# Performance work log

Measured on AMD Instinct MI355X. Metric: run time of the kernel, lower is better.

## Reference

```python
import jax, jax.numpy as jnp
import numpy as np

EPROJS = 512
ODIM = 600
DLAYERS = 2
DUNITS = 512
EMBED_DIM = 512
JOINT_DIM = 512
BLANK = 0


def setup_inputs() -> dict:
    key = jax.random.key(0)
    ks = jax.random.split(key, 20)
    B, T, U = 16, 200, 64
    s_d = 1.0 / np.sqrt(DUNITS)
    s_e = 1.0 / np.sqrt(EPROJS)
    s_j = 1.0 / np.sqrt(JOINT_DIM)
    inp = {
        "hs_pad": jax.random.normal(ks[0], (B, T, EPROJS), dtype=jnp.float32),
        "ys_in_pad": jax.random.randint(ks[1], (B, U), 0, ODIM),
        "embed_table": jax.random.normal(ks[2], (ODIM, EMBED_DIM), dtype=jnp.float32).at[BLANK].set(0.0),
        # LSTMCell layer 0: input EMBED_DIM -> DUNITS (gates i,f,g,o stacked => 4*DUNITS)
        "W_ih0": jax.random.uniform(ks[3], (4 * DUNITS, EMBED_DIM), minval=-s_d, maxval=s_d),
        "W_hh0": jax.random.uniform(ks[4], (4 * DUNITS, DUNITS), minval=-s_d, maxval=s_d),
        "b_ih0": jax.random.uniform(ks[5], (4 * DUNITS,), minval=-s_d, maxval=s_d),
        "b_hh0": jax.random.uniform(ks[6], (4 * DUNITS,), minval=-s_d, maxval=s_d),
        # LSTMCell layer 1: DUNITS -> DUNITS
        "W_ih1": jax.random.uniform(ks[7], (4 * DUNITS, DUNITS), minval=-s_d, maxval=s_d),
        "W_hh1": jax.random.uniform(ks[8], (4 * DUNITS, DUNITS), minval=-s_d, maxval=s_d),
        "b_ih1": jax.random.uniform(ks[9], (4 * DUNITS,), minval=-s_d, maxval=s_d),
        "b_hh1": jax.random.uniform(ks[10], (4 * DUNITS,), minval=-s_d, maxval=s_d),
        # joint network
        "W_enc": jax.random.uniform(ks[11], (JOINT_DIM, EPROJS), minval=-s_e, maxval=s_e),
        "b_enc": jax.random.uniform(ks[12], (JOINT_DIM,), minval=-s_e, maxval=s_e),
        "W_dec": jax.random.uniform(ks[13], (JOINT_DIM, DUNITS), minval=-s_d, maxval=s_d),
        "W_out": jax.random.uniform(ks[14], (ODIM, JOINT_DIM), minval=-s_j, maxval=s_j),
        "b_out": jax.random.uniform(ks[15], (ODIM,), minval=-s_j, maxval=s_j),
    }
    return inp


def _lstm_cell(x, h, c, W_ih, W_hh, b_ih, b_hh):
    gates = x @ W_ih.T + b_ih + h @ W_hh.T + b_hh  # (B, 4*D)
    i, f, g, o = jnp.split(gates, 4, axis=-1)
    c_new = jax.nn.sigmoid(f) * c + jax.nn.sigmoid(i) * jnp.tanh(g)
    h_new = jax.nn.sigmoid(o) * jnp.tanh(c_new)
    return h_new, c_new


def _decode(eys, W_ih0, W_hh0, b_ih0, b_hh0, W_ih1, W_hh1, b_ih1, b_hh1):
    # eys: (B, U, E). Sequential 2-layer LSTM over U via scan.
    B = eys.shape[0]
    z = jnp.zeros((B, DUNITS), dtype=eys.dtype)
    carry0 = (z, z, z, z)  # h0, c0, h1, c1

    def step(carry, ey):
        h0, c0, h1, c1 = carry
        h0, c0 = _lstm_cell(ey, h0, c0, W_ih0, W_hh0, b_ih0, b_hh0)
        h1, c1 = _lstm_cell(h0, h1, c1, W_ih1, W_hh1, b_ih1, b_hh1)
        return (h0, c0, h1, c1), h1

    _, h_dec = jax.lax.scan(step, carry0, jnp.swapaxes(eys, 0, 1))  # (U, B, D)
    return jnp.swapaxes(h_dec, 0, 1)  # (B, U, D)


def reference(hs_pad, ys_in_pad, embed_table, W_ih0, W_hh0, b_ih0, b_hh0,
              W_ih1, W_hh1, b_ih1, b_hh1, W_enc, b_enc, W_dec, W_out, b_out):
    eys = embed_table[ys_in_pad]  # (B, U, E); dropout = identity at p=0
    h_dec = _decode(eys, W_ih0, W_hh0, b_ih0, b_hh0, W_ih1, W_hh1, b_ih1, b_hh1)
    # Joint: project BEFORE broadcasting (thin GEMMs), then broadcast-add.
    enc_p = hs_pad @ W_enc.T + b_enc            # (B, T, J)
    dec_p = h_dec @ W_dec.T                     # (B, U, J)
    z = jnp.tanh(enc_p[:, :, None, :] + dec_p[:, None, :, :])  # (B, T, U, J)
    return z @ W_out.T + b_out                  # (B, T, U, odim)
```

## Files before the change

kernel.cpp:

```cpp
#include <hip/hip_runtime.h>
#include <hip/hip_bf16.h>
#include <stdint.h>

#define DEVI __device__ __forceinline__

typedef unsigned short u16;
typedef __attribute__((ext_vector_type(8))) short short8;
typedef __attribute__((ext_vector_type(4))) float f32x4;
typedef __attribute__((ext_vector_type(16))) float f32x16;

DEVI u16 f2bf(float f) {
  union { float f; uint32_t u; } v; v.f = f;
  return (u16)((v.u + 0x7fffu + ((v.u >> 16) & 1u)) >> 16);
}
DEVI float tanh_c(float x) {
  float e = __expf(x + x);
  float r = __builtin_amdgcn_rcpf(e + 1.0f);
  return __builtin_fmaf(-2.0f, r, 1.0f);
}
DEVI float sigm(float x) { return __builtin_amdgcn_rcpf(1.0f + __expf(-x)); }
DEVI uint32_t tj2(float a, float b) {
  float ea = __expf(a + a), eb = __expf(b + b);
  float ta = __builtin_fmaf(-2.0f, __builtin_amdgcn_rcpf(ea + 1.0f), 1.0f);
  float tb = __builtin_fmaf(-2.0f, __builtin_amdgcn_rcpf(eb + 1.0f), 1.0f);
  union { __hip_bfloat162 h; uint32_t u; } cv;
  cv.h = __float22bfloat162_rn(make_float2(ta, tb));
  return cv.u;
}

__global__ void prep_kernel(
    const float* __restrict__ W_ih0, const float* __restrict__ W_hh0,
    const float* __restrict__ W_ih1, const float* __restrict__ W_hh1,
    const float* __restrict__ W_enc, const float* __restrict__ W_dec,
    const float* __restrict__ W_out, const float* __restrict__ embed,
    const float* __restrict__ hs_pad,
    const float* __restrict__ b_ih0, const float* __restrict__ b_hh0,
    const float* __restrict__ b_ih1, const float* __restrict__ b_hh1,
    const float* __restrict__ b_out,
    u16* __restrict__ Wih0b, u16* __restrict__ Whh0b,
    u16* __restrict__ Wih1b, u16* __restrict__ Whh1b,
    u16* __restrict__ Wencb, u16* __restrict__ Wdecb,
    u16* __restrict__ embedb, u16* __restrict__ hsb,
    u16* __restrict__ Wshufb,
    float* __restrict__ bsum0, float* __restrict__ bsum1, float* __restrict__ boutp)
{
  const int c1 = 1048576, c2 = 2097152, c3 = 3145728, c4 = 4194304;
  const int c5 = 4456448, c6 = 4718592, c7 = 5025792, c8 = 6664192;
  const int c9 = 6991872, c10 = 6993920, c11 = 6995968, c12 = 6996608;
  for (int i = blockIdx.x * blockDim.x + threadIdx.x; i < c12; i += gridDim.x * blockDim.x) {
    if (i < c1)       Wih0b[i]      = f2bf(W_ih0[i]);
    else if (i < c2)  Whh0b[i - c1] = f2bf(W_hh0[i - c1]);
    else if (i < c3)  Wih1b[i - c2] = f2bf(W_ih1[i - c2]);
    else if (i < c4)  Whh1b[i - c3] = f2bf(W_hh1[i - c3]);
    else if (i < c5)  Wencb[i - c4] = f2bf(W_enc[i - c4]);
    else if (i < c6)  Wdecb[i - c5] = f2bf(W_dec[i - c5]);
    else if (i < c7)  embedb[i - c6] = f2bf(embed[i - c6]);
    else if (i < c8)  hsb[i - c7]   = f2bf(hs_pad[i - c7]);
    else if (i < c9) {
      int e = i - c8;
      int kc = e / 10240, r = e % 10240;
      int tile = r >> 9, r2 = r & 511;
      int lane = r2 >> 3, ii = r2 & 7;
      int n = tile * 32 + (lane & 31);
      int k = kc * 16 + ((lane >> 5) << 3) + ii;
      Wshufb[e] = (n < 600) ? f2bf(W_out[n * 512 + k]) : (u16)0;
    }
    else if (i < c10) { int n = i - c9;  bsum0[n] = b_ih0[n] + b_hh0[n]; }
    else if (i < c11) { int n = i - c10; bsum1[n] = b_ih1[n] + b_hh1[n]; }
    else              { int n = i - c11; boutp[n] = (n < 600) ? b_out[n] : 0.0f; }
  }
}

__global__ __launch_bounds__(256) void gemm_bf16(
    const u16* __restrict__ A, const u16* __restrict__ B,
    const int* __restrict__ ys, const float* __restrict__ bias,
    float* __restrict__ out, int N, int mode)
{
  int tid = threadIdx.x, wv = tid >> 6, l = tid & 63;
  int m0 = blockIdx.x * 64, n0 = blockIdx.y * 64;
  int row = m0 + wv * 16 + (l & 15);
  const u16* arow;
  if (mode == 1) { int uu = row >> 4, bb = row & 15; arow = A + (size_t)ys[bb * 64 + uu] * 512; }
  else           arow = A + (size_t)row * 512;
  int kof = (l >> 4) * 8;
  arow += kof;
  const u16* br = B + (size_t)(n0 + (l & 15)) * 512 + kof;
  f32x4 a0 = {0.f,0.f,0.f,0.f}, a1 = a0, a2 = a0, a3 = a0;
  for (int kk = 0; kk < 512; kk += 32) {
    short8 av = *(const short8*)(arow + kk);
    short8 b0 = *(const short8*)(br + kk);
    short8 b1 = *(const short8*)(br + 8192 + kk);
    short8 b2 = *(const short8*)(br + 16384 + kk);
    short8 b3 = *(const short8*)(br + 24576 + kk);
    a0 = __builtin_amdgcn_mfma_f32_16x16x32_bf16(av, b0, a0, 0, 0, 0);
    a1 = __builtin_amdgcn_mfma_f32_16x16x32_bf16(av, b1, a1, 0, 0, 0);
    a2 = __builtin_amdgcn_mfma_f32_16x16x32_bf16(av, b2, a2, 0, 0, 0);
    a3 = __builtin_amdgcn_mfma_f32_16x16x32_bf16(av, b3, a3, 0, 0, 0);
  }
  int col = l & 15, rb = m0 + wv * 16 + (l >> 4) * 4;
  f32x4 accs[4] = {a0, a1, a2, a3};
#pragma unroll
  for (int g = 0; g < 4; ++g) {
    int n = n0 + g * 16 + col;
    float bs = bias ? bias[n] : 0.0f;
#pragma unroll
    for (int i2 = 0; i2 < 4; ++i2)
      out[(size_t)(rb + i2) * N + n] = accs[g][i2] + bs;
  }
}

#define L0WG 32
#define NWGT 96

DEVI short8 ald16(const u16* p) {
  union { unsigned long long q[2]; short8 v; } u;
  u.q[0] = __hip_atomic_load((unsigned long long*)p,       __ATOMIC_RELAXED, __HIP_MEMORY_SCOPE_AGENT);
  u.q[1] = __hip_atomic_load((unsigned long long*)(p + 4), __ATOMIC_RELAXED, __HIP_MEMORY_SCOPE_AGENT);
  return u.v;
}
DEVI void waitflags(const int* f0, const int* f1, int n0, int n1) {
  if (threadIdx.x < 64) {
    int l = threadIdx.x;
    for (;;) {
      int a = __hip_atomic_load((int*)(f0 + (l & 31) * 16), __ATOMIC_RELAXED, __HIP_MEMORY_SCOPE_AGENT);
      int b = __hip_atomic_load((int*)(f1 + l * 16),        __ATOMIC_RELAXED, __HIP_MEMORY_SCOPE_AGENT);
      if (__all(a >= n0 && b >= n1)) break;
      __builtin_amdgcn_s_sleep(1);
    }
    __builtin_amdgcn_fence(__ATOMIC_ACQUIRE, "agent");
  }
  __syncthreads();
}
DEVI void postflag(int* slot, int val) {
  __syncthreads();
  if (threadIdx.x == 0) {
    asm volatile("s_waitcnt vmcnt(0)" ::: "memory");
    __hip_atomic_store(slot, val, __ATOMIC_RELAXED, __HIP_MEMORY_SCOPE_AGENT);
  }
}
DEVI const u16* haddr(const u16* base, int slot, int k, int b) {
  return base + slot * 8192 + (k >> 4) * 256 + b * 16 + (k & 15);
}
DEVI void hstore(u16* base, int idx, u16 mine, int tid) {
  int other = __shfl_xor((int)mine, 1);
  if (!(tid & 1)) {
    uint32_t pkv = (uint32_t)mine | (((uint32_t)other & 0xffffu) << 16);
    __hip_atomic_store((uint32_t*)(base + idx), pkv, __ATOMIC_RELAXED, __HIP_MEMORY_SCOPE_AGENT);
  }
}

__global__ __launch_bounds__(256) void lstm_kernel(
    const float* __restrict__ Xg0,
    const u16* __restrict__ Whh0, const u16* __restrict__ Wih1, const u16* __restrict__ Whh1,
    const float* __restrict__ bsum1,
    u16* __restrict__ h0b, u16* __restrict__ h1b,
    u16* __restrict__ Hdec,
    int* __restrict__ flags0, int* __restrict__ flags1)
{
  __shared__ float red[16][256];
  const int bid = blockIdx.x, tid = threadIdx.x;
  const int wv = tid >> 6, l = tid & 63;
  const int lb = l & 15, kof = (l >> 4) * 8;
  const int drb = (l >> 4) * 4;

  if (bid < L0WG) {
    const int be = tid >> 4, je = tid & 15, jg = (bid << 4) + je;
    short8 breg[16];
#pragma unroll
    for (int g = 0; g < 4; ++g) {
      const u16* bp = Whh0 + (size_t)(g * 512 + bid * 16 + lb) * 512 + wv * 128 + kof;
#pragma unroll
      for (int ks = 0; ks < 4; ++ks)
        breg[g * 4 + ks] = *(const short8*)(bp + ks * 32);
    }
    float c0 = 0.f;
    for (int t = 0; t < 64; ++t) {
      const float* xg = Xg0 + (size_t)((t << 4) + be) * 2048 + jg;
      float x0 = xg[0], x1 = xg[512], x2 = xg[1024], x3 = xg[1536];
      waitflags(flags0, flags1, t, (t > 7) ? (t - 7) : 0);
      const int rs = (t + 7) & 7;
      f32x4 g0 = {0.f,0.f,0.f,0.f}, g1 = g0, g2 = g0, g3 = g0;
#pragma unroll
      for (int ks = 0; ks < 4; ++ks) {
        int kk = wv * 128 + ks * 32 + kof;
        short8 av = ald16(haddr(h0b, rs, kk, lb));
        g0 = __builtin_amdgcn_mfma_f32_16x16x32_bf16(av, breg[0 * 4 + ks], g0, 0, 0, 0);
        g1 = __builtin_amdgcn_mfma_f32_16x16x32_bf16(av, breg[1 * 4 + ks], g1, 0, 0, 0);
        g2 = __builtin_amdgcn_mfma_f32_16x16x32_bf16(av, breg[2 * 4 + ks], g2, 0, 0, 0);
        g3 = __builtin_amdgcn_mfma_f32_16x16x32_bf16(av, breg[3 * 4 + ks], g3, 0, 0, 0);
      }
      f32x4 gs[4] = {g0, g1, g2, g3};
#pragma unroll
      for (int g = 0; g < 4; ++g)
#pragma unroll
        for (int i2 = 0; i2 < 4; ++i2)
          red[wv * 4 + g][(drb + i2) * 16 + lb] = gs[g][i2];
      __syncthreads();
      {
        float s0 = 0, s1 = 0, s2 = 0, s3 = 0;
#pragma unroll
        for (int v2 = 0; v2 < 4; ++v2) {
          s0 += red[v2 * 4 + 0][be * 16 + je]; s1 += red[v2 * 4 + 1][be * 16 + je];
          s2 += red[v2 * 4 + 2][be * 16 + je]; s3 += red[v2 * 4 + 3][be * 16 + je];
        }
        float gi = s0 + x0, gf = s1 + x1, gg = s2 + x2, go = s3 + x3;
        float I = sigm(gi), F = sigm(gf), G = tanh_c(gg), O = sigm(go);
        c0 = F * c0 + I * G;
        float h0 = O * tanh_c(c0);
        hstore(h0b, ((t & 7) * 32 + bid) * 256 + (tid & ~1), f2bf(h0), tid);
      }
      postflag(flags0 + bid * 16, t + 1);
    }
  } else {
    const int v = bid - L0WG;
    const u16* base0 = (wv < 2) ? Wih1 : Whh1;
    const int kbase = (wv & 1) * 256;
    short8 breg[16];
#pragma unroll
    for (int tt = 0; tt < 2; ++tt) {
      int c = tt * 16 + lb, gate = c >> 3, du = c & 7;
      const u16* bp = base0 + (size_t)(gate * 512 + v * 8 + du) * 512 + kbase + kof;
#pragma unroll
      for (int ks = 0; ks < 8; ++ks)
        breg[tt * 8 + ks] = *(const short8*)(bp + ks * 32);
    }
    float bs0 = 0, bs1 = 0, bs2 = 0, bs3 = 0, c1 = 0.f;
    if (tid < 128) {
      int du = tid & 7, ju = v * 8 + du;
      bs0 = bsum1[ju]; bs1 = bsum1[512 + ju]; bs2 = bsum1[1024 + ju]; bs3 = bsum1[1536 + ju];
    }
    for (int t = 0; t < 64; ++t) {
      waitflags(flags0, flags1, t + 1, t);
      const u16* hsrc = (wv < 2) ? (h0b + (t & 7) * 8192) : (h1b + ((t + 7) & 7) * 8192);
      f32x4 g0 = {0.f,0.f,0.f,0.f}, g1 = g0;
#pragma unroll
      for (int ks = 0; ks < 8; ++ks) {
        int kk = kbase + ks * 32 + kof;
        short8 av = ald16(hsrc + (kk >> 4) * 256 + lb * 16 + (kk & 15));
        g0 = __builtin_amdgcn_mfma_f32_16x16x32_bf16(av, breg[0 * 8 + ks], g0, 0, 0, 0);
        g1 = __builtin_amdgcn_mfma_f32_16x16x32_bf16(av, breg[1 * 8 + ks], g1, 0, 0, 0);
      }
#pragma unroll
      for (int i2 = 0; i2 < 4; ++i2) {
        red[wv * 2 + 0][(drb + i2) * 16 + lb] = g0[i2];
        red[wv * 2 + 1][(drb + i2) * 16 + lb] = g1[i2];
      }
      __syncthreads();
      u16 hb = 0; int be = 0, ju = 0;
      if (tid < 128) {
        be = tid >> 3; int du = tid & 7; ju = v * 8 + du;
        float sg[4] = {bs0, bs1, bs2, bs3};
#pragma unroll
        for (int g = 0; g < 4; ++g) {
          int c = g * 8 + du, tt = c >> 4, cc = c & 15;
          float acc = 0.f;
#pragma unroll
          for (int w2 = 0; w2 < 4; ++w2) acc += red[w2 * 2 + tt][be * 16 + cc];
          sg[g] += acc;
        }
        float I = sigm(sg[0]), F = sigm(sg[1]), G = tanh_c(sg[2]), O = sigm(sg[3]);
        c1 = F * c1 + I * G;
        float h1v = O * tanh_c(c1);
        hb = f2bf(h1v);
        int idx = ((t & 7) * 32 + (ju >> 4)) * 256 + be * 16 + (ju & 15);
        hstore(h1b, idx & ~1, hb, tid);
      }
      postflag(flags1 + v * 16, t + 1);
      if (tid < 128) Hdec[(size_t)((t << 4) + be) * 512 + ju] = hb;
    }
  }
}

__global__ __launch_bounds__(256) void joint_kernel(
    const float* __restrict__ enc_p,
    const float* __restrict__ dec_p,
    const u16* __restrict__ Wshuf,
    const float* __restrict__ boutp,
    float* __restrict__ out)
{
  __shared__ int4 wlds[2][1280];
  __shared__ int4 zlds[2][256];
  int bid = blockIdx.x;
  int b = bid / 400, rem = bid % 400;
  int tb = rem / 8, rem2 = rem % 8;
  int ub = rem2 >> 1, nh = rem2 & 1;
  int tid = threadIdx.x, wv = tid >> 6, l = tid & 63;
  int mv = wv >> 1, nv = wv & 1;
  int ln31 = l & 31, lh = l >> 5;
  const int tile0 = nv * 5;
  f32x16 acc[5];
#pragma unroll
  for (int j = 0; j < 5; ++j) {
    float bv = boutp[nh * 320 + (tile0 + j) * 32 + ln31];
#pragma unroll
    for (int g = 0; g < 16; ++g) acc[j][g] = bv;
  }
  int zr = tid & 63, zg = tid >> 6;
  const float* er = enc_p + (size_t)(b * 200 + tb * 4 + (zr >> 4)) * 512 + zg * 8;
  const float* dr = dec_p + (size_t)((ub * 16 + (zr & 15)) * 16 + b) * 512 + zg * 8;
  const int zslot = ((zg >> 1) * 2 + (zr >> 5)) * 64 + ((zg & 1) << 5) + (zr & 31);
  const int4* gW = (const int4*)Wshuf;
  const int nhof = nh * 640;
  const int L0 = tid, L1 = 256 + tid, L2 = 512 + tid + ((tid >= 128) ? 640 : 0),
            L3 = 1408 + tid, L4 = 1664 + tid;
  const int S2 = 512 + tid;

  {
    int4 w0 = gW[nhof + L0], w1 = gW[nhof + L1], w2 = gW[nhof + L2],
         w3 = gW[nhof + L3], w4 = gW[nhof + L4];
    float4 e0 = *(const float4*)(er),     e1 = *(const float4*)(er + 4);
    float4 d0 = *(const float4*)(dr),     d1 = *(const float4*)(dr + 4);
    int4 pk;
    pk.x = (int)tj2(e0.x + d0.x, e0.y + d0.y);
    pk.y = (int)tj2(e0.z + d0.z, e0.w + d0.w);
    pk.z = (int)tj2(e1.x + d1.x, e1.y + d1.y);
    pk.w = (int)tj2(e1.z + d1.z, e1.w + d1.w);
    zlds[0][zslot] = pk;
    wlds[0][tid] = w0; wlds[0][256 + tid] = w1; wlds[0][S2] = w2;
    wlds[0][768 + tid] = w3; wlds[0][1024 + tid] = w4;
    __syncthreads();
  }

  for (int c = 0; c < 16; ++c) {
    const int cur = c & 1, nxt = cur ^ 1;
    const bool pf = (c < 15);
    int4 w0, w1, w2, w3, w4;
    float4 e0, e1, d0, d1;
    if (pf) {
      const int cb = (c + 1) * 2560 + nhof;
      w0 = gW[cb + L0]; w1 = gW[cb + L1]; w2 = gW[cb + L2];
      w3 = gW[cb + L3]; w4 = gW[cb + L4];
      int k0 = (c + 1) * 32;
      e0 = *(const float4*)(er + k0);     e1 = *(const float4*)(er + k0 + 4);
      d0 = *(const float4*)(dr + k0);     d1 = *(const float4*)(dr + k0 + 4);
    }
#pragma unroll
    for (int ks = 0; ks < 2; ++ks) {
      short8 aA = *(const short8*)&zlds[cur][(ks * 2 + mv) * 64 + l];
#pragma unroll
      for (int j = 0; j < 5; ++j) {
        short8 bw = *(const short8*)&wlds[cur][ks * 640 + (tile0 + j) * 64 + l];
        acc[j] = __builtin_amdgcn_mfma_f32_32x32x16_bf16(aA, bw, acc[j], 0, 0, 0);
      }
    }
    if (pf) {
      wlds[nxt][tid] = w0; wlds[nxt][256 + tid] = w1; wlds[nxt][S2] = w2;
      wlds[nxt][768 + tid] = w3; wlds[nxt][1024 + tid] = w4;
      int4 pk;
      pk.x = (int)tj2(e0.x + d0.x, e0.y + d0.y);
      pk.y = (int)tj2(e0.z + d0.z, e0.w + d0.w);
      pk.z = (int)tj2(e1.x + d1.x, e1.y + d1.y);
      pk.w = (int)tj2(e1.z + d1.z, e1.w + d1.w);
      zlds[nxt][zslot] = pk;
    }
    __syncthreads();
  }

#pragma unroll
  for (int j = 0; j < 5; ++j) {
    int n = nh * 320 + (tile0 + j) * 32 + ln31;
    if (n < 600) {
      int rbase = mv * 32 + 4 * lh;
#pragma unroll
      for (int g = 0; g < 16; ++g) {
        int r = rbase + (g & 3) + ((g >> 2) << 3);
        int tt = tb * 4 + (r >> 4), uu = ub * 16 + (r & 15);
        __builtin_nontemporal_store(
            acc[j][g], &out[(size_t)((b * 200 + tt) * 64 + uu) * 600 + n]);
      }
    }
  }
}

extern "C" void kernel_launch(void* const* d_in, const int* in_sizes, int n_in,
                              void* d_out, int out_size, void* d_ws, size_t ws_size,
                              hipStream_t stream) {
  const float* hs_pad = (const float*)d_in[0];
  const int*   ys     = (const int*)d_in[1];
  const float* embed  = (const float*)d_in[2];
  const float* W_ih0  = (const float*)d_in[3];
  const float* W_hh0  = (const float*)d_in[4];
  const float* b_ih0  = (const float*)d_in[5];
  const float* b_hh0  = (const float*)d_in[6];
  const float* W_ih1  = (const float*)d_in[7];
  const float* W_hh1  = (const float*)d_in[8];
  const float* b_ih1  = (const float*)d_in[9];
  const float* b_hh1  = (const float*)d_in[10];
  const float* W_enc  = (const float*)d_in[11];
  const float* b_enc  = (const float*)d_in[12];
  const float* W_dec  = (const float*)d_in[13];
  const float* W_out  = (const float*)d_in[14];
  const float* b_out  = (const float*)d_in[15];
  float* out = (float*)d_out;

  uint8_t* ws = (uint8_t*)d_ws;
  size_t off = 0;
  auto alloc = [&](size_t bytes) -> void* {
    void* p = ws + off;
    off = (off + bytes + 255) & ~(size_t)255;
    return p;
  };
  int* flags0   = (int*)alloc(2048);
  int* flags1   = (int*)alloc(4096);
  u16* h0buf    = (u16*)alloc(8 * 32 * 256 * 2);
  u16* h1buf    = (u16*)alloc(8 * 32 * 256 * 2);
  u16* Hdec     = (u16*)alloc(64 * 16 * 512 * 2);
  float* Xg0    = (float*)alloc(1024 * 2048 * 4);
  float* enc_p  = (float*)alloc(3200 * 512 * 4);
  float* dec_p  = (float*)alloc(1024 * 512 * 4);
  u16* Wih0b    = (u16*)alloc(2048 * 512 * 2);
  u16* Whh0b    = (u16*)alloc(2048 * 512 * 2);
  u16* Wih1b    = (u16*)alloc(2048 * 512 * 2);
  u16* Whh1b    = (u16*)alloc(2048 * 512 * 2);
  u16* Wencb    = (u16*)alloc(512 * 512 * 2);
  u16* Wdecb    = (u16*)alloc(512 * 512 * 2);
  u16* embedb   = (u16*)alloc(600 * 512 * 2);
  u16* hsb      = (u16*)alloc(3200 * 512 * 2);
  u16* Wshufb   = (u16*)alloc(32 * 20 * 64 * 8 * 2);
  float* bsum0  = (float*)alloc(2048 * 4);
  float* bsum1  = (float*)alloc(2048 * 4);
  float* boutp  = (float*)alloc(640 * 4);

  (void)hipMemsetAsync(d_ws, 0, 2048 + 4096 + 131072 + 131072, stream);

  prep_kernel<<<2048, 256, 0, stream>>>(
      W_ih0, W_hh0, W_ih1, W_hh1, W_enc, W_dec, W_out, embed, hs_pad,
      b_ih0, b_hh0, b_ih1, b_hh1, b_out,
      Wih0b, Whh0b, Wih1b, Whh1b, Wencb, Wdecb, embedb, hsb, Wshufb,
      bsum0, bsum1, boutp);

  dim3 g1(16, 32);
  gemm_bf16<<<g1, 256, 0, stream>>>(embedb, Wih0b, ys, bsum0, Xg0, 2048, 1);
  dim3 g2(50, 8);
  gemm_bf16<<<g2, 256, 0, stream>>>(hsb, Wencb, nullptr, b_enc, enc_p, 512, 0);
  lstm_kernel<<<NWGT, 256, 0, stream>>>(Xg0, Whh0b, Wih1b, Whh1b, bsum1,
                                        h0buf, h1buf, Hdec, flags0, flags1);
  dim3 g3(16, 8);
  gemm_bf16<<<g3, 256, 0, stream>>>(Hdec, Wdecb, nullptr, nullptr, dec_p, 512, 0);
  joint_kernel<<<6400, 256, 0, stream>>>(enc_p, dec_p, Wshufb, boutp, out);
}
```

Before: 604.9 us.

## Replace flag-based LSTM synchronization with tagged hidden-state words in full-length ring

The persistent LSTM kernel no longer posts and polls per-workgroup flags. Each packed bf16 pair of the hidden state is now written as a 64-bit word carrying its timestep tag, and consumers spin until every loaded word has the expected tag. This removes the separate flag round trip, the acquire fence and one barrier per step from the recurrent critical path. In exchange the h buffers are twice as wide, hold all 65 timesteps instead of an 8-slot ring, and need a larger memset, and correctness relies on each 64-bit atomic store being seen whole.

```diff
diff --git a/kernel.cpp b/kernel.cpp
--- a/kernel.cpp
+++ b/kernel.cpp
@@ -5,6 +5,7 @@
 #define DEVI __device__ __forceinline__
 
 typedef unsigned short u16;
+typedef unsigned long long u64;
 typedef __attribute__((ext_vector_type(8))) short short8;
 typedef __attribute__((ext_vector_type(4))) float f32x4;
 typedef __attribute__((ext_vector_type(16))) float f32x16;
@@ -112,40 +113,24 @@
 #define L0WG 32
 #define NWGT 96
 
-DEVI short8 ald16(const u16* p) {
-  union { unsigned long long q[2]; short8 v; } u;
-  u.q[0] = __hip_atomic_load((unsigned long long*)p,       __ATOMIC_RELAXED, __HIP_MEMORY_SCOPE_AGENT);
-  u.q[1] = __hip_atomic_load((unsigned long long*)(p + 4), __ATOMIC_RELAXED, __HIP_MEMORY_SCOPE_AGENT);
-  return u.v;
-}
-DEVI void waitflags(const int* f0, const int* f1, int n0, int n1) {
-  if (threadIdx.x < 64) {
-    int l = threadIdx.x;
-    for (;;) {
-      int a = __hip_atomic_load((int*)(f0 + (l & 31) * 16), __ATOMIC_RELAXED, __HIP_MEMORY_SCOPE_AGENT);
-      int b = __hip_atomic_load((int*)(f1 + l * 16),        __ATOMIC_RELAXED, __HIP_MEMORY_SCOPE_AGENT);
-      if (__all(a >= n0 && b >= n1)) break;
-      __builtin_amdgcn_s_sleep(1);
-    }
-    __builtin_amdgcn_fence(__ATOMIC_ACQUIRE, "agent");
-  }
-  __syncthreads();
-}
-DEVI void postflag(int* slot, int val) {
-  __syncthreads();
-  if (threadIdx.x == 0) {
-    asm volatile("s_waitcnt vmcnt(0)" ::: "memory");
-    __hip_atomic_store(slot, val, __ATOMIC_RELAXED, __HIP_MEMORY_SCOPE_AGENT);
-  }
-}
-DEVI const u16* haddr(const u16* base, int slot, int k, int b) {
-  return base + slot * 8192 + (k >> 4) * 256 + b * 16 + (k & 15);
-}
-DEVI void hstore(u16* base, int idx, u16 mine, int tid) {
+DEVI bool tagld4(const u64* p, uint32_t tag, short8* out) {
+  u64 q0 = __hip_atomic_load(p + 0, __ATOMIC_RELAXED, __HIP_MEMORY_SCOPE_AGENT);
+  u64 q1 = __hip_atomic_load(p + 1, __ATOMIC_RELAXED, __HIP_MEMORY_SCOPE_AGENT);
+  u64 q2 = __hip_atomic_load(p + 2, __ATOMIC_RELAXED, __HIP_MEMORY_SCOPE_AGENT);
+  u64 q3 = __hip_atomic_load(p + 3, __ATOMIC_RELAXED, __HIP_MEMORY_SCOPE_AGENT);
+  union { int4 d; short8 s; } u;
+  u.d = make_int4((int)(uint32_t)q0, (int)(uint32_t)q1,
+                  (int)(uint32_t)q2, (int)(uint32_t)q3);
+  *out = u.s;
+  return ((uint32_t)(q0 >> 32) == tag) & ((uint32_t)(q1 >> 32) == tag)
+       & ((uint32_t)(q2 >> 32) == tag) & ((uint32_t)(q3 >> 32) == tag);
+}
+DEVI void hst64(u64* base, int idx, u16 mine, int tid, uint32_t tag) {
   int other = __shfl_xor((int)mine, 1);
   if (!(tid & 1)) {
-    uint32_t pkv = (uint32_t)mine | (((uint32_t)other & 0xffffu) << 16);
-    __hip_atomic_store((uint32_t*)(base + idx), pkv, __ATOMIC_RELAXED, __HIP_MEMORY_SCOPE_AGENT);
+    u64 v = ((u64)tag << 32) |
+            (u64)(uint32_t)((uint32_t)mine | (((uint32_t)other & 0xffffu) << 16));
+    __hip_atomic_store(base + idx, v, __ATOMIC_RELAXED, __HIP_MEMORY_SCOPE_AGENT);
   }
 }
 
@@ -153,15 +138,15 @@
     const float* __restrict__ Xg0,
     const u16* __restrict__ Whh0, const u16* __restrict__ Wih1, const u16* __restrict__ Whh1,
     const float* __restrict__ bsum1,
-    u16* __restrict__ h0b, u16* __restrict__ h1b,
-    u16* __restrict__ Hdec,
-    int* __restrict__ flags0, int* __restrict__ flags1)
+    u64* __restrict__ h0r, u64* __restrict__ h1r,
+    u16* __restrict__ Hdec)
 {
   __shared__ float red[16][256];
   const int bid = blockIdx.x, tid = threadIdx.x;
   const int wv = tid >> 6, l = tid & 63;
   const int lb = l & 15, kof = (l >> 4) * 8;
   const int drb = (l >> 4) * 4;
+  const int pof = ((kof >> 4)) * 128 + lb * 8 + ((kof & 8) >> 1);
 
   if (bid < L0WG) {
     const int be = tid >> 4, je = tid & 15, jg = (bid << 4) + je;
@@ -173,22 +158,38 @@
       for (int ks = 0; ks < 4; ++ks)
         breg[g * 4 + ks] = *(const short8*)(bp + ks * 32);
     }
+    const int koff = wv * 8 * 128 + pof;
     float c0 = 0.f;
     for (int t = 0; t < 64; ++t) {
       const float* xg = Xg0 + (size_t)((t << 4) + be) * 2048 + jg;
       float x0 = xg[0], x1 = xg[512], x2 = xg[1024], x3 = xg[1536];
-      waitflags(flags0, flags1, t, (t > 7) ? (t - 7) : 0);
-      const int rs = (t + 7) & 7;
+      const u64* hp = h0r + (size_t)t * 4096 + koff;
+      short8 av0, av1, av2, av3;
+      for (;;) {
+        bool ok = tagld4(hp +   0, (uint32_t)t, &av0);
+        ok &=     tagld4(hp + 256, (uint32_t)t, &av1);
+        ok &=     tagld4(hp + 512, (uint32_t)t, &av2);
+        ok &=     tagld4(hp + 768, (uint32_t)t, &av3);
+        if (__all(ok)) break;
+        __builtin_amdgcn_s_sleep(1);
+      }
       f32x4 g0 = {0.f,0.f,0.f,0.f}, g1 = g0, g2 = g0, g3 = g0;
-#pragma unroll
-      for (int ks = 0; ks < 4; ++ks) {
-        int kk = wv * 128 + ks * 32 + kof;
-        short8 av = ald16(haddr(h0b, rs, kk, lb));
-        g0 = __builtin_amdgcn_mfma_f32_16x16x32_bf16(av, breg[0 * 4 + ks], g0, 0, 0, 0);
-        g1 = __builtin_amdgcn_mfma_f32_16x16x32_bf16(av, breg[1 * 4 + ks], g1, 0, 0, 0);
-        g2 = __builtin_amdgcn_mfma_f32_16x16x32_bf16(av, breg[2 * 4 + ks], g2, 0, 0, 0);
-        g3 = __builtin_amdgcn_mfma_f32_16x16x32_bf16(av, breg[3 * 4 + ks], g3, 0, 0, 0);
-      }
+      g0 = __builtin_amdgcn_mfma_f32_16x16x32_bf16(av0, breg[0],  g0, 0, 0, 0);
+      g1 = __builtin_amdgcn_mfma_f32_16x16x32_bf16(av0, breg[4],  g1, 0, 0, 0);
+      g2 = __builtin_amdgcn_mfma_f32_16x16x32_bf16(av0, breg[8],  g2, 0, 0, 0);
+      g3 = __builtin_amdgcn_mfma_f32_16x16x32_bf16(av0, breg[12], g3, 0, 0, 0);
+      g0 = __builtin_amdgcn_mfma_f32_16x16x32_bf16(av1, breg[1],  g0, 0, 0, 0);
+      g1 = __builtin_amdgcn_mfma_f32_16x16x32_bf16(av1, breg[5],  g1, 0, 0, 0);
+      g2 = __builtin_amdgcn_mfma_f32_16x16x32_bf16(av1, breg[9],  g2, 0, 0, 0);
+      g3 = __builtin_amdgcn_mfma_f32_16x16x32_bf16(av1, breg[13], g3, 0, 0, 0);
+      g0 = __builtin_amdgcn_mfma_f32_16x16x32_bf16(av2, breg[2],  g0, 0, 0, 0);
+      g1 = __builtin_amdgcn_mfma_f32_16x16x32_bf16(av2, breg[6],  g1, 0, 0, 0);
+      g2 = __builtin_amdgcn_mfma_f32_16x16x32_bf16(av2, breg[10], g2, 0, 0, 0);
+      g3 = __builtin_amdgcn_mfma_f32_16x16x32_bf16(av2, breg[14], g3, 0, 0, 0);
+      g0 = __builtin_amdgcn_mfma_f32_16x16x32_bf16(av3, breg[3],  g0, 0, 0, 0);
+      g1 = __builtin_amdgcn_mfma_f32_16x16x32_bf16(av3, breg[7],  g1, 0, 0, 0);
+      g2 = __builtin_amdgcn_mfma_f32_16x16x32_bf16(av3, breg[11], g2, 0, 0, 0);
+      g3 = __builtin_amdgcn_mfma_f32_16x16x32_bf16(av3, breg[15], g3, 0, 0, 0);
       f32x4 gs[4] = {g0, g1, g2, g3};
 #pragma unroll
       for (int g = 0; g < 4; ++g)
@@ -207,9 +208,10 @@
         float I = sigm(gi), F = sigm(gf), G = tanh_c(gg), O = sigm(go);
         c0 = F * c0 + I * G;
         float h0 = O * tanh_c(c0);
-        hstore(h0b, ((t & 7) * 32 + bid) * 256 + (tid & ~1), f2bf(h0), tid);
-      }
-      postflag(flags0 + bid * 16, t + 1);
+        hst64(h0r, (t + 1) * 4096 + bid * 128 + be * 8 + (je >> 1),
+              f2bf(h0), tid, (uint32_t)(t + 1));
+      }
+      __syncthreads();
     }
   } else {
     const int v = bid - L0WG;
@@ -229,16 +231,25 @@
       int du = tid & 7, ju = v * 8 + du;
       bs0 = bsum1[ju]; bs1 = bsum1[512 + ju]; bs2 = bsum1[1024 + ju]; bs3 = bsum1[1536 + ju];
     }
+    const int koff = (kbase >> 4) * 128 + pof;
     for (int t = 0; t < 64; ++t) {
-      waitflags(flags0, flags1, t + 1, t);
-      const u16* hsrc = (wv < 2) ? (h0b + (t & 7) * 8192) : (h1b + ((t + 7) & 7) * 8192);
+      const u64* hp = ((wv < 2) ? (h0r + (size_t)(t + 1) * 4096)
+                                : (h1r + (size_t)t * 4096)) + koff;
+      const uint32_t etag = (wv < 2) ? (uint32_t)(t + 1) : (uint32_t)t;
+      short8 av[8];
+      for (;;) {
+        bool ok = true;
+#pragma unroll
+        for (int ks = 0; ks < 8; ++ks)
+          ok &= tagld4(hp + ks * 256, etag, &av[ks]);
+        if (__all(ok)) break;
+        __builtin_amdgcn_s_sleep(1);
+      }
       f32x4 g0 = {0.f,0.f,0.f,0.f}, g1 = g0;
 #pragma unroll
       for (int ks = 0; ks < 8; ++ks) {
-        int kk = kbase + ks * 32 + kof;
-        short8 av = ald16(hsrc + (kk >> 4) * 256 + lb * 16 + (kk & 15));
-        g0 = __builtin_amdgcn_mfma_f32_16x16x32_bf16(av, breg[0 * 8 + ks], g0, 0, 0, 0);
-        g1 = __builtin_amdgcn_mfma_f32_16x16x32_bf16(av, breg[1 * 8 + ks], g1, 0, 0, 0);
+        g0 = __builtin_amdgcn_mfma_f32_16x16x32_bf16(av[ks], breg[0 * 8 + ks], g0, 0, 0, 0);
+        g1 = __builtin_amdgcn_mfma_f32_16x16x32_bf16(av[ks], breg[1 * 8 + ks], g1, 0, 0, 0);
       }
 #pragma unroll
       for (int i2 = 0; i2 < 4; ++i2) {
@@ -262,11 +273,11 @@
         c1 = F * c1 + I * G;
         float h1v = O * tanh_c(c1);
         hb = f2bf(h1v);
-        int idx = ((t & 7) * 32 + (ju >> 4)) * 256 + be * 16 + (ju & 15);
-        hstore(h1b, idx & ~1, hb, tid);
-      }
-      postflag(flags1 + v * 16, t + 1);
-      if (tid < 128) Hdec[(size_t)((t << 4) + be) * 512 + ju] = hb;
+        hst64(h1r, (t + 1) * 4096 + (ju >> 4) * 128 + be * 8 + ((ju & 15) >> 1),
+              hb, tid, (uint32_t)(t + 1));
+        Hdec[(size_t)((t << 4) + be) * 512 + ju] = hb;
+      }
+      __syncthreads();
     }
   }
 }
@@ -400,10 +411,8 @@
     off = (off + bytes + 255) & ~(size_t)255;
     return p;
   };
-  int* flags0   = (int*)alloc(2048);
-  int* flags1   = (int*)alloc(4096);
-  u16* h0buf    = (u16*)alloc(8 * 32 * 256 * 2);
-  u16* h1buf    = (u16*)alloc(8 * 32 * 256 * 2);
+  u64* h0ring   = (u64*)alloc(65 * 4096 * 8);
+  u64* h1ring   = (u64*)alloc(65 * 4096 * 8);
   u16* Hdec     = (u16*)alloc(64 * 16 * 512 * 2);
   float* Xg0    = (float*)alloc(1024 * 2048 * 4);
   float* enc_p  = (float*)alloc(3200 * 512 * 4);
@@ -421,7 +430,7 @@
   float* bsum1  = (float*)alloc(2048 * 4);
   float* boutp  = (float*)alloc(640 * 4);
 
-  (void)hipMemsetAsync(d_ws, 0, 2048 + 4096 + 131072 + 131072, stream);
+  (void)hipMemsetAsync(d_ws, 0, 2 * 65 * 4096 * 8, stream);
 
   prep_kernel<<<2048, 256, 0, stream>>>(
       W_ih0, W_hh0, W_ih1, W_hh1, W_enc, W_dec, W_out, embed, hs_pad,
@@ -434,7 +443,7 @@
   dim3 g2(50, 8);
   gemm_bf16<<<g2, 256, 0, stream>>>(hsb, Wencb, nullptr, b_enc, enc_p, 512, 0);
   lstm_kernel<<<NWGT, 256, 0, stream>>>(Xg0, Whh0b, Wih1b, Whh1b, bsum1,
-                                        h0buf, h1buf, Hdec, flags0, flags1);
+                                        h0ring, h1ring, Hdec);
   dim3 g3(16, 8);
   gemm_bf16<<<g3, 256, 0, stream>>>(Hdec, Wdecb, nullptr, nullptr, dec_p, 512, 0);
   joint_kernel<<<6400, 256, 0, stream>>>(enc_p, dec_p, Wshufb, boutp, out);
```

Measured after the change: 615.3 us. No clear change (+1.7%).
